# Optimization experiments

Hardware: AMD Instinct MI355X
Metric: run time of the kernel (lower is better)

The kernel has to match this reference:

```python
import jax, jax.numpy as jnp
import numpy as np
import math

N_EMBD = 768
N_HEAD = 12


def setup_inputs() -> dict:
    key = jax.random.key(0)
    k1, k2, k3, k4, k5 = jax.random.split(key, 5)
    B, T, C = 2, 4096, N_EMBD
    s_in = 1.0 / math.sqrt(C)
    x = jax.random.normal(k1, (B, T, C), dtype=jnp.float32)
    W_attn = jax.random.normal(k2, (C, 3 * C), dtype=jnp.float32) * s_in
    b_attn = jax.random.normal(k3, (3 * C,), dtype=jnp.float32) * 0.01
    W_proj = jax.random.normal(k4, (C, C), dtype=jnp.float32) * s_in
    b_proj = jax.random.normal(k5, (C,), dtype=jnp.float32) * 0.01
    return {"x": x, "W_attn": W_attn, "b_attn": b_attn, "W_proj": W_proj, "b_proj": b_proj}


def reference(x, W_attn, b_attn, W_proj, b_proj):
    B, T, C = x.shape
    H = N_HEAD
    D = C // H  # head dim
    qkv = x @ W_attn + b_attn  # [B,T,3C]
    # NOTE: original splits as (k, q, v) in that order
    k, q, v = jnp.split(qkv, 3, axis=2)
    # [B,T,C] -> [B,H,T,D]
    k = k.reshape(B, T, H, D).transpose(0, 2, 1, 3)
    q = q.reshape(B, T, H, D).transpose(0, 2, 1, 3)
    v = v.reshape(B, T, H, D).transpose(0, 2, 1, 3)
    scale = 1.0 / math.sqrt(D)
    scores = jnp.einsum('bhqd,bhkd->bhqk', q, k) * scale  # [B,H,T,T]
    causal = jnp.tril(jnp.ones((T, T), dtype=bool))
    scores = jnp.where(causal, scores, jnp.float32(-jnp.inf))
    weights = jax.nn.softmax(scores, axis=-1)  # attn dropout p=0 (eval)
    out = jnp.einsum('bhqk,bhkd->bhqd', weights, v)  # [B,H,T,D]
    out = out.transpose(0, 2, 1, 3).reshape(B, T, C)
    out = out @ W_proj + b_proj  # resid dropout p=0 (eval)
    return out
```

## Files before the change

### kernel.cpp

```cpp
#include <hip/hip_runtime.h>


#define TSEQ 4096
#define NH   12
#define HD   64
#define CEMB 768

typedef __attribute__((ext_vector_type(8))) short s8v;
typedef __attribute__((ext_vector_type(4))) float f32x4;

__device__ __forceinline__ ushort f2bf(float f) {
  union { float f; unsigned u; } x; x.f = f;
  unsigned u = x.u;
  u += 0x7fffu + ((u >> 16) & 1);
  return (ushort)(u >> 16);
}

__device__ __forceinline__ void gload16(const void* gsrc, void* ldst) {
  __builtin_amdgcn_global_load_lds(
      (const __attribute__((address_space(1))) unsigned int*)gsrc,
      (__attribute__((address_space(3))) unsigned int*)ldst, 16, 0, 0);
}

__global__ void cvt_x_kernel(const float* __restrict__ x, ushort* __restrict__ xb, int n4) {
  int i = blockIdx.x * blockDim.x + threadIdx.x;
  const int stride = gridDim.x * blockDim.x;
  for (; i < n4; i += stride) {
    float4 v = ((const float4*)x)[i];
    ushort4 o;
    o.x = f2bf(v.x); o.y = f2bf(v.y); o.z = f2bf(v.z); o.w = f2bf(v.w);
    ((ushort4*)xb)[i] = o;
  }
}

__global__ void transpose_cvt_kernel(const float* __restrict__ W, ushort* __restrict__ WT,
                                     int R, int Cn) {
  __shared__ ushort tile[32][33];
  const int bx = blockIdx.x * 32;
  const int by = blockIdx.y * 32;
  const int tx = threadIdx.x;
  const int ty = threadIdx.y;
#pragma unroll
  for (int i = ty; i < 32; i += 8)
    tile[i][tx] = f2bf(W[(size_t)(by + i) * Cn + bx + tx]);
  __syncthreads();
#pragma unroll
  for (int i = ty; i < 32; i += 8)
    WT[(size_t)(bx + i) * R + by + tx] = tile[tx][i];
}

#define QSC 0.18033688011112042f

template <int EPI>
__global__ void gemm128_kernel(const ushort* __restrict__ A, const ushort* __restrict__ Bt,
                               const float* __restrict__ bias,
                               ushort* __restrict__ oq, ushort* __restrict__ ok,
                               ushort* __restrict__ ovT, float* __restrict__ fout,
                               int Ktot) {
  __shared__ ushort lA[128 * 32];
  __shared__ ushort lB[128 * 32];
  const int tid = threadIdx.x;
  const int bm = blockIdx.x, bn = blockIdx.y;
  const int wid = tid >> 6, lane = tid & 63;
  const int wr = wid >> 1, wc = wid & 1;
  const int lr = lane & 15, hi = lane >> 4;

  const f32x4 fzero = {0.f, 0.f, 0.f, 0.f};
  f32x4 acc[4][4];
#pragma unroll
  for (int m = 0; m < 4; ++m)
#pragma unroll
    for (int n = 0; n < 4; ++n) acc[m][n] = fzero;

  const int g0 = tid, g1 = tid + 256;
  const int rA0 = bm * 128 + (g0 >> 2), kO0 = (g0 & 3) * 8;
  const int rA1 = bm * 128 + (g1 >> 2), kO1 = (g1 & 3) * 8;
  const int rB0 = bn * 128 + (g0 >> 2);
  const int rB1 = bn * 128 + (g1 >> 2);

  for (int kt = 0; kt < Ktot; kt += 32) {
    __syncthreads();
    gload16(A + (size_t)rA0 * Ktot + kt + kO0, &lA[g0 * 8]);
    gload16(A + (size_t)rA1 * Ktot + kt + kO1, &lA[g1 * 8]);
    gload16(Bt + (size_t)rB0 * Ktot + kt + kO0, &lB[g0 * 8]);
    gload16(Bt + (size_t)rB1 * Ktot + kt + kO1, &lB[g1 * 8]);
    __syncthreads();
    s8v av[4], bv[4];
#pragma unroll
    for (int m = 0; m < 4; ++m)
      av[m] = *(const s8v*)&lA[(wr * 64 + m * 16 + lr) * 32 + hi * 8];
#pragma unroll
    for (int n = 0; n < 4; ++n)
      bv[n] = *(const s8v*)&lB[(wc * 64 + n * 16 + lr) * 32 + hi * 8];
#pragma unroll
    for (int m = 0; m < 4; ++m)
#pragma unroll
      for (int n = 0; n < 4; ++n)
        acc[m][n] = __builtin_amdgcn_mfma_f32_16x16x32_bf16(av[m], bv[n], acc[m][n], 0, 0, 0);
  }

  if (EPI == 0) {
    const int which = bn / 6;
#pragma unroll
    for (int n = 0; n < 4; ++n) {
      const int col = bn * 128 + wc * 64 + n * 16 + lr;
      const float bsv = bias[col];
      const int c = col - which * CEMB;
      const int h = c >> 6, d = c & 63;
#pragma unroll
      for (int m = 0; m < 4; ++m) {
        const int row0 = bm * 128 + wr * 64 + m * 16 + hi * 4;
        const int b = row0 >> 12, t0 = row0 & 4095;
        if (which == 2) {
          uint2 w;
          w.x = (uint)f2bf(acc[m][n][0] + bsv) | ((uint)f2bf(acc[m][n][1] + bsv) << 16);
          w.y = (uint)f2bf(acc[m][n][2] + bsv) | ((uint)f2bf(acc[m][n][3] + bsv) << 16);
          *(uint2*)(ovT + ((size_t)(b * NH + h) * HD + d) * TSEQ + t0) = w;
        } else {
#pragma unroll
          for (int r = 0; r < 4; ++r) {
            const float val = acc[m][n][r] + bsv;
            const size_t idx = ((size_t)(b * NH + h) * TSEQ + t0 + r) * HD + d;
            if (which == 0) ok[idx] = f2bf(val);
            else            oq[idx] = f2bf(val * QSC);
          }
        }
      }
    }
  } else {
#pragma unroll
    for (int n = 0; n < 4; ++n) {
      const int col = bn * 128 + wc * 64 + n * 16 + lr;
      const float bsv = bias[col];
#pragma unroll
      for (int m = 0; m < 4; ++m) {
        const int row0 = bm * 128 + wr * 64 + m * 16 + hi * 4;
#pragma unroll
        for (int r = 0; r < 4; ++r)
          fout[(size_t)(row0 + r) * CEMB + col] = acc[m][n][r] + bsv;
      }
    }
  }
}

__global__ void attn_kernel(const ushort* __restrict__ qb, const ushort* __restrict__ kb,
                            const ushort* __restrict__ vT, ushort* __restrict__ ao) {
  __shared__ ushort lK[2][4096];
  __shared__ ushort lV[2][4096];
  __shared__ ushort lP[4][2048];

  const int bh = blockIdx.y;
  const int b = bh / NH, h = bh % NH;
  const int tid = threadIdx.x;
  const int wid = tid >> 6, lane = tid & 63;
  const int lr = lane & 15, hi = lane >> 4;
  const int qchunk = gridDim.x - 1 - blockIdx.x;
  const int wq = qchunk * 128 + wid * 32;

  const ushort* qpb = qb + ((size_t)bh * TSEQ) * HD;
  s8v qfr[2][2];
#pragma unroll
  for (int qf = 0; qf < 2; ++qf)
#pragma unroll
    for (int kh = 0; kh < 2; ++kh)
      qfr[qf][kh] = *(const s8v*)(qpb + (size_t)(wq + qf * 16 + lr) * HD + kh * 32 + hi * 8);

  const ushort* kpb = kb + (size_t)bh * TSEQ * HD;
  const ushort* vtb = vT + (size_t)bh * HD * TSEQ;

  const f32x4 fzero = {0.f, 0.f, 0.f, 0.f};
  f32x4 ot[4][2];
#pragma unroll
  for (int df = 0; df < 4; ++df)
#pragma unroll
    for (int qf = 0; qf < 2; ++qf) ot[df][qf] = fzero;
  float m_run[2] = {-1e30f, -1e30f};
  float l_run[2] = {0.f, 0.f};

  const int nt = qchunk * 2 + 2;
  const int sgc0 = wid * 64 + lane, sgc1 = sgc0 + 256;
  const int sr0 = sgc0 >> 3, sb0 = (sgc0 & 7) ^ (sr0 & 7);
  const int sr1 = sgc1 >> 3, sb1 = (sgc1 & 7) ^ (sr1 & 7);

#define STAGE(buf, kv0)                                               \
  do {                                                                \
    gload16(kpb + (size_t)((kv0) + sr0) * HD + sb0 * 8, &lK[buf][sgc0 * 8]); \
    gload16(vtb + (size_t)sr0 * TSEQ + (kv0) + sb0 * 8, &lV[buf][sgc0 * 8]); \
    gload16(kpb + (size_t)((kv0) + sr1) * HD + sb1 * 8, &lK[buf][sgc1 * 8]); \
    gload16(vtb + (size_t)sr1 * TSEQ + (kv0) + sb1 * 8, &lV[buf][sgc1 * 8]); \
  } while (0)

#define QFWORK(qf, QMIN)                                                     \
  do {                                                                       \
    if (kv0 + 63 > (QMIN)) {                                                 \
      _Pragma("unroll") for (int kvf = 0; kvf < 4; ++kvf)                    \
        _Pragma("unroll") for (int r = 0; r < 4; ++r)                        \
          if (kv0 + kvf * 16 + hi * 4 + r > (QMIN) + lr)                     \
            st[kvf][qf][r] = -1e30f;                                         \
    }                                                                        \
    float pmax = -1e30f;                                                     \
    _Pragma("unroll") for (int kvf = 0; kvf < 4; ++kvf)                      \
      _Pragma("unroll") for (int r = 0; r < 4; ++r)                          \
        pmax = fmaxf(pmax, st[kvf][qf][r]);                                  \
    pmax = fmaxf(pmax, __shfl_xor(pmax, 16));                                \
    pmax = fmaxf(pmax, __shfl_xor(pmax, 32));                                \
    const float m_new = fmaxf(m_run[qf], pmax);                              \
    const float scq = __builtin_amdgcn_exp2f(m_run[qf] - m_new);             \
    float psum = 0.f;                                                        \
    _Pragma("unroll") for (int kvf = 0; kvf < 4; ++kvf)                      \
      _Pragma("unroll") for (int r = 0; r < 4; ++r) {                        \
        const float p = __builtin_amdgcn_exp2f(st[kvf][qf][r] - m_new);      \
        st[kvf][qf][r] = p;                                                  \
        psum += p;                                                           \
      }                                                                      \
    psum += __shfl_xor(psum, 16);                                            \
    psum += __shfl_xor(psum, 32);                                            \
    l_run[qf] = l_run[qf] * scq + psum;                                      \
    m_run[qf] = m_new;                                                       \
    _Pragma("unroll") for (int df = 0; df < 4; ++df) {                       \
      ot[df][qf][0] *= scq; ot[df][qf][1] *= scq;                            \
      ot[df][qf][2] *= scq; ot[df][qf][3] *= scq;                            \
    }                                                                        \
    const int rowb = ((qf) * 16 + lr) * 128;                                 \
    _Pragma("unroll") for (int kvf = 0; kvf < 4; ++kvf) {                    \
      uint wlo, whi;                                                         \
      asm("v_cvt_pk_bf16_f32 %0, %1, %2"                                     \
          : "=v"(wlo) : "v"(st[kvf][qf][0]), "v"(st[kvf][qf][1]));           \
      asm("v_cvt_pk_bf16_f32 %0, %1, %2"                                     \
          : "=v"(whi) : "v"(st[kvf][qf][2]), "v"(st[kvf][qf][3]));           \
      uint2 w; w.x = wlo; w.y = whi;                                         \
      *(uint2*)((char*)pw + rowb + ((kvf * 32 + hi * 8) ^ sw)) = w;          \
    }                                                                        \
  } while (0)

  STAGE(0, 0);
  asm volatile("s_waitcnt vmcnt(0)" ::: "memory");
  __syncthreads();

  int cur = 0;
  const int sw = (lr & 7) << 4;
  ushort* pw = lP[wid];

  for (int t = 0; t < nt; ++t) {
    const int kv0 = t * 64;
    if (t + 1 < nt) STAGE(cur ^ 1, kv0 + 64);

    if (kv0 <= wq + 31) {
      const char* lKb = (const char*)lK[cur];
      const char* lVb = (const char*)lV[cur];
      f32x4 st[4][2];
      __builtin_amdgcn_s_setprio(1);
#pragma unroll
      for (int kvf = 0; kvf < 4; ++kvf) {
        const int row = kvf * 16 + lr;
        const s8v a0 = *(const s8v*)(lKb + row * 128 + ((hi * 16) ^ sw));
        const s8v a1 = *(const s8v*)(lKb + row * 128 + ((64 + hi * 16) ^ sw));
#pragma unroll
        for (int qf = 0; qf < 2; ++qf) {
          f32x4 s = fzero;
          s = __builtin_amdgcn_mfma_f32_16x16x32_bf16(a0, qfr[qf][0], s, 0, 0, 0);
          s = __builtin_amdgcn_mfma_f32_16x16x32_bf16(a1, qfr[qf][1], s, 0, 0, 0);
          st[kvf][qf] = s;
        }
      }
      __builtin_amdgcn_s_setprio(0);

      QFWORK(1, wq + 16);
      QFWORK(0, wq);

      asm volatile("s_waitcnt lgkmcnt(0)" ::: "memory");
      __builtin_amdgcn_sched_barrier(0);

      __builtin_amdgcn_s_setprio(1);
#pragma unroll
      for (int s = 0; s < 2; ++s) {
        s8v vf[4];
#pragma unroll
        for (int df = 0; df < 4; ++df) {
          const int row = df * 16 + lr;
          vf[df] = *(const s8v*)(lVb + row * 128 + ((s * 64 + hi * 16) ^ sw));
        }
#pragma unroll
        for (int qf = 0; qf < 2; ++qf) {
          const s8v pf = *(const s8v*)((char*)pw + (qf * 16 + lr) * 128 + ((s * 64 + hi * 16) ^ sw));
#pragma unroll
          for (int df = 0; df < 4; ++df)
            ot[df][qf] = __builtin_amdgcn_mfma_f32_16x16x32_bf16(vf[df], pf, ot[df][qf], 0, 0, 0);
        }
      }
      __builtin_amdgcn_s_setprio(0);
    }

    asm volatile("s_waitcnt vmcnt(0)" ::: "memory");
    __syncthreads();
    cur ^= 1;
  }

#pragma unroll
  for (int qf = 0; qf < 2; ++qf) {
    const float inv_l = 1.f / l_run[qf];
    ushort* op = ao + ((size_t)(b * TSEQ + wq + qf * 16 + lr)) * CEMB + h * HD + hi * 4;
#pragma unroll
    for (int df = 0; df < 4; ++df) {
      const float o0 = ot[df][qf][0] * inv_l, o1 = ot[df][qf][1] * inv_l;
      const float o2 = ot[df][qf][2] * inv_l, o3 = ot[df][qf][3] * inv_l;
      uint wlo, whi;
      asm("v_cvt_pk_bf16_f32 %0, %1, %2" : "=v"(wlo) : "v"(o0), "v"(o1));
      asm("v_cvt_pk_bf16_f32 %0, %1, %2" : "=v"(whi) : "v"(o2), "v"(o3));
      uint2 w; w.x = wlo; w.y = whi;
      *(uint2*)(op + df * 16) = w;
    }
  }
#undef STAGE
#undef QFWORK
}

extern "C" void kernel_launch(void* const* d_in, const int* in_sizes, int n_in,
                              void* d_out, int out_size, void* d_ws, size_t ws_size,
                              hipStream_t stream) {
  const float* x      = (const float*)d_in[0];
  const float* W_attn = (const float*)d_in[1];
  const float* b_attn = (const float*)d_in[2];
  const float* W_proj = (const float*)d_in[3];
  const float* b_proj = (const float*)d_in[4];
  float* out = (float*)d_out;

  char* ws = (char*)d_ws;
  ushort* xb  = (ushort*)(ws + 0);
  ushort* WaT = (ushort*)(ws + 12582912);
  ushort* WpT = (ushort*)(ws + 16121856);
  ushort* qbf = (ushort*)(ws + 17301504);
  ushort* kbf = (ushort*)(ws + 29884416);
  ushort* vTb = (ushort*)(ws + 55050240);

  cvt_x_kernel<<<dim3(2048), dim3(256), 0, stream>>>(x, xb, (2 * TSEQ * CEMB) / 4);
  transpose_cvt_kernel<<<dim3(72, 24), dim3(32, 8), 0, stream>>>(W_attn, WaT, CEMB, 3 * CEMB);
  transpose_cvt_kernel<<<dim3(24, 24), dim3(32, 8), 0, stream>>>(W_proj, WpT, CEMB, CEMB);
  gemm128_kernel<0><<<dim3(64, 18), dim3(256), 0, stream>>>(xb, WaT, b_attn,
                                                            qbf, kbf, vTb, nullptr, CEMB);
  attn_kernel<<<dim3(32, 24), dim3(256), 0, stream>>>(qbf, kbf, vTb, xb);
  gemm128_kernel<1><<<dim3(64, 6), dim3(256), 0, stream>>>(xb, WpT, b_proj,
                                                           nullptr, nullptr, nullptr, out, CEMB);
}
```

Before: 335.6 us.

## Widen GEMM K-tile with swizzled LDS, vectorize epilogues, add lazy softmax rescale

The QKV and projection GEMM now stages 64-wide K tiles into XOR-swizzled LDS, which halves the barriers per K and avoids bank conflicts. For the non-V outputs it swaps the MFMA operand order so each lane holds four consecutive columns, which allows float4 bias loads and vectorized 8-byte or 16-byte stores. The attention softmax skips rescaling the running max and accumulator unless the new max exceeds the old by more than 8 (a log2-domain threshold), cutting per-tile multiplies. The lazy rescale lets unnormalized exponentials grow up to 2^8, which slightly affects bf16 rounding of P.

```diff
diff --git a/kernel.cpp b/kernel.cpp
--- a/kernel.cpp
+++ b/kernel.cpp
@@ -57,13 +57,15 @@
                                ushort* __restrict__ oq, ushort* __restrict__ ok,
                                ushort* __restrict__ ovT, float* __restrict__ fout,
                                int Ktot) {
-  __shared__ ushort lA[128 * 32];
-  __shared__ ushort lB[128 * 32];
+  __shared__ ushort lA[128 * 64];
+  __shared__ ushort lB[128 * 64];
   const int tid = threadIdx.x;
   const int bm = blockIdx.x, bn = blockIdx.y;
   const int wid = tid >> 6, lane = tid & 63;
   const int wr = wid >> 1, wc = wid & 1;
   const int lr = lane & 15, hi = lane >> 4;
+  const int which = (EPI == 0) ? (bn / 6) : 1;
+  const bool vblk = (EPI == 0) && (which == 2);
 
   const f32x4 fzero = {0.f, 0.f, 0.f, 0.f};
   f32x4 acc[4][4];
@@ -72,72 +74,103 @@
 #pragma unroll
     for (int n = 0; n < 4; ++n) acc[m][n] = fzero;
 
-  const int g0 = tid, g1 = tid + 256;
-  const int rA0 = bm * 128 + (g0 >> 2), kO0 = (g0 & 3) * 8;
-  const int rA1 = bm * 128 + (g1 >> 2), kO1 = (g1 & 3) * 8;
-  const int rB0 = bn * 128 + (g0 >> 2);
-  const int rB1 = bn * 128 + (g1 >> 2);
-
-  for (int kt = 0; kt < Ktot; kt += 32) {
+  int srow[4], soff[4];
+#pragma unroll
+  for (int i = 0; i < 4; ++i) {
+    const int c = tid + 256 * i;
+    srow[i] = c >> 3;
+    soff[i] = ((c & 7) ^ (srow[i] & 7)) * 8;
+  }
+
+  for (int kt = 0; kt < Ktot; kt += 64) {
     __syncthreads();
-    gload16(A + (size_t)rA0 * Ktot + kt + kO0, &lA[g0 * 8]);
-    gload16(A + (size_t)rA1 * Ktot + kt + kO1, &lA[g1 * 8]);
-    gload16(Bt + (size_t)rB0 * Ktot + kt + kO0, &lB[g0 * 8]);
-    gload16(Bt + (size_t)rB1 * Ktot + kt + kO1, &lB[g1 * 8]);
+#pragma unroll
+    for (int i = 0; i < 4; ++i) {
+      gload16(A + (size_t)(bm * 128 + srow[i]) * Ktot + kt + soff[i], &lA[(tid + 256 * i) * 8]);
+      gload16(Bt + (size_t)(bn * 128 + srow[i]) * Ktot + kt + soff[i], &lB[(tid + 256 * i) * 8]);
+    }
     __syncthreads();
-    s8v av[4], bv[4];
-#pragma unroll
-    for (int m = 0; m < 4; ++m)
-      av[m] = *(const s8v*)&lA[(wr * 64 + m * 16 + lr) * 32 + hi * 8];
-#pragma unroll
-    for (int n = 0; n < 4; ++n)
-      bv[n] = *(const s8v*)&lB[(wc * 64 + n * 16 + lr) * 32 + hi * 8];
-#pragma unroll
-    for (int m = 0; m < 4; ++m)
-#pragma unroll
-      for (int n = 0; n < 4; ++n)
-        acc[m][n] = __builtin_amdgcn_mfma_f32_16x16x32_bf16(av[m], bv[n], acc[m][n], 0, 0, 0);
+#pragma unroll
+    for (int kk = 0; kk < 2; ++kk) {
+      s8v av[4], bv[4];
+#pragma unroll
+      for (int m = 0; m < 4; ++m) {
+        const int row = wr * 64 + m * 16 + lr;
+        av[m] = *(const s8v*)((const char*)lA + row * 128 + ((kk * 64 + hi * 16) ^ ((row & 7) << 4)));
+      }
+#pragma unroll
+      for (int n = 0; n < 4; ++n) {
+        const int row = wc * 64 + n * 16 + lr;
+        bv[n] = *(const s8v*)((const char*)lB + row * 128 + ((kk * 64 + hi * 16) ^ ((row & 7) << 4)));
+      }
+      if (vblk) {
+#pragma unroll
+        for (int m = 0; m < 4; ++m)
+#pragma unroll
+          for (int n = 0; n < 4; ++n)
+            acc[m][n] = __builtin_amdgcn_mfma_f32_16x16x32_bf16(av[m], bv[n], acc[m][n], 0, 0, 0);
+      } else {
+#pragma unroll
+        for (int m = 0; m < 4; ++m)
+#pragma unroll
+          for (int n = 0; n < 4; ++n)
+            acc[m][n] = __builtin_amdgcn_mfma_f32_16x16x32_bf16(bv[n], av[m], acc[m][n], 0, 0, 0);
+      }
+    }
   }
 
   if (EPI == 0) {
-    const int which = bn / 6;
-#pragma unroll
-    for (int n = 0; n < 4; ++n) {
-      const int col = bn * 128 + wc * 64 + n * 16 + lr;
-      const float bsv = bias[col];
-      const int c = col - which * CEMB;
-      const int h = c >> 6, d = c & 63;
-#pragma unroll
-      for (int m = 0; m < 4; ++m) {
-        const int row0 = bm * 128 + wr * 64 + m * 16 + hi * 4;
-        const int b = row0 >> 12, t0 = row0 & 4095;
-        if (which == 2) {
+    if (vblk) {
+#pragma unroll
+      for (int n = 0; n < 4; ++n) {
+        const int col = bn * 128 + wc * 64 + n * 16 + lr;
+        const float bsv = bias[col];
+        const int c = col - 2 * CEMB;
+        const int h = c >> 6, d = c & 63;
+#pragma unroll
+        for (int m = 0; m < 4; ++m) {
+          const int row0 = bm * 128 + wr * 64 + m * 16 + hi * 4;
+          const int b = row0 >> 12, t0 = row0 & 4095;
           uint2 w;
           w.x = (uint)f2bf(acc[m][n][0] + bsv) | ((uint)f2bf(acc[m][n][1] + bsv) << 16);
           w.y = (uint)f2bf(acc[m][n][2] + bsv) | ((uint)f2bf(acc[m][n][3] + bsv) << 16);
           *(uint2*)(ovT + ((size_t)(b * NH + h) * HD + d) * TSEQ + t0) = w;
-        } else {
-#pragma unroll
-          for (int r = 0; r < 4; ++r) {
-            const float val = acc[m][n][r] + bsv;
-            const size_t idx = ((size_t)(b * NH + h) * TSEQ + t0 + r) * HD + d;
-            if (which == 0) ok[idx] = f2bf(val);
-            else            oq[idx] = f2bf(val * QSC);
-          }
+        }
+      }
+    } else {
+#pragma unroll
+      for (int n = 0; n < 4; ++n) {
+        const int col0 = bn * 128 + wc * 64 + n * 16 + hi * 4;
+        const float4 b4 = *(const float4*)&bias[col0];
+        const int cl = col0 - which * CEMB;
+        const int h = cl >> 6, d = cl & 63;
+#pragma unroll
+        for (int m = 0; m < 4; ++m) {
+          const int tg = bm * 128 + wr * 64 + m * 16 + lr;
+          const int b = tg >> 12, t = tg & 4095;
+          float v0 = acc[m][n][0] + b4.x, v1 = acc[m][n][1] + b4.y;
+          float v2 = acc[m][n][2] + b4.z, v3 = acc[m][n][3] + b4.w;
+          if (which == 1) { v0 *= QSC; v1 *= QSC; v2 *= QSC; v3 *= QSC; }
+          uint2 w;
+          w.x = (uint)f2bf(v0) | ((uint)f2bf(v1) << 16);
+          w.y = (uint)f2bf(v2) | ((uint)f2bf(v3) << 16);
+          ushort* dst = (which == 0) ? ok : oq;
+          *(uint2*)(dst + ((size_t)(b * NH + h) * TSEQ + t) * HD + d) = w;
         }
       }
     }
   } else {
 #pragma unroll
     for (int n = 0; n < 4; ++n) {
-      const int col = bn * 128 + wc * 64 + n * 16 + lr;
-      const float bsv = bias[col];
+      const int col0 = bn * 128 + wc * 64 + n * 16 + hi * 4;
+      const float4 b4 = *(const float4*)&bias[col0];
 #pragma unroll
       for (int m = 0; m < 4; ++m) {
-        const int row0 = bm * 128 + wr * 64 + m * 16 + hi * 4;
-#pragma unroll
-        for (int r = 0; r < 4; ++r)
-          fout[(size_t)(row0 + r) * CEMB + col] = acc[m][n][r] + bsv;
+        const int tg = bm * 128 + wr * 64 + m * 16 + lr;
+        float4 o;
+        o.x = acc[m][n][0] + b4.x; o.y = acc[m][n][1] + b4.y;
+        o.z = acc[m][n][2] + b4.z; o.w = acc[m][n][3] + b4.w;
+        *(float4*)&fout[(size_t)tg * CEMB + col0] = o;
       }
     }
   }
@@ -204,23 +237,27 @@
         pmax = fmaxf(pmax, st[kvf][qf][r]);                                  \
     pmax = fmaxf(pmax, __shfl_xor(pmax, 16));                                \
     pmax = fmaxf(pmax, __shfl_xor(pmax, 32));                                \
-    const float m_new = fmaxf(m_run[qf], pmax);                              \
-    const float scq = __builtin_amdgcn_exp2f(m_run[qf] - m_new);             \
+    if (!__all(pmax <= m_run[qf] + 8.f)) {                                   \
+      const float m_new = fmaxf(m_run[qf], pmax);                            \
+      const float scq = __builtin_amdgcn_exp2f(m_run[qf] - m_new);           \
+      l_run[qf] *= scq;                                                      \
+      m_run[qf] = m_new;                                                     \
+      _Pragma("unroll") for (int df = 0; df < 4; ++df) {                     \
+        ot[df][qf][0] *= scq; ot[df][qf][1] *= scq;                          \
+        ot[df][qf][2] *= scq; ot[df][qf][3] *= scq;                          \
+      }                                                                      \
+    }                                                                        \
+    const float mref = m_run[qf];                                            \
     float psum = 0.f;                                                        \
     _Pragma("unroll") for (int kvf = 0; kvf < 4; ++kvf)                      \
       _Pragma("unroll") for (int r = 0; r < 4; ++r) {                        \
-        const float p = __builtin_amdgcn_exp2f(st[kvf][qf][r] - m_new);      \
+        const float p = __builtin_amdgcn_exp2f(st[kvf][qf][r] - mref);       \
         st[kvf][qf][r] = p;                                                  \
         psum += p;                                                           \
       }                                                                      \
     psum += __shfl_xor(psum, 16);                                            \
     psum += __shfl_xor(psum, 32);                                            \
-    l_run[qf] = l_run[qf] * scq + psum;                                      \
-    m_run[qf] = m_new;                                                       \
-    _Pragma("unroll") for (int df = 0; df < 4; ++df) {                       \
-      ot[df][qf][0] *= scq; ot[df][qf][1] *= scq;                            \
-      ot[df][qf][2] *= scq; ot[df][qf][3] *= scq;                            \
-    }                                                                        \
+    l_run[qf] += psum;                                                       \
     const int rowb = ((qf) * 16 + lr) * 128;                                 \
     _Pragma("unroll") for (int kvf = 0; kvf < 4; ++kvf) {                    \
       uint wlo, whi;                                                         \
```

After: 584.3 us. 74.1% more time.
